# Optimization experiments

Hardware: AMD Instinct MI355X
Metric: run time of the kernel (lower is better)

Reference implementation:

```python
import jax, jax.numpy as jnp
import numpy as np

# Config (Qwen3-4B-like, from ModelConfig defaults in source)
B = 32          # batch = number of decode requests = total_q
H = 32          # num_attention_heads
KVH = 8         # num_key_value_heads
G = H // KVH    # num_kv_groups = 4
D = 128         # head_dim
HID = 2560      # hidden_size
PS = 16         # page_size
MAXP = 128      # max_num_pages per request
NPAGES = B * MAXP   # 4096 pages in pool
MAXKV = MAXP * PS   # 2048
THETA = 5000000.0
EPS = 1e-6


def setup_inputs() -> dict:
    key = jax.random.key(0)
    ks = jax.random.split(key, 12)
    x = jax.random.normal(ks[0], (1, B, HID), dtype=jnp.float32)
    Wq = jax.random.normal(ks[1], (H * D, HID), dtype=jnp.float32) * 0.02
    Wk = jax.random.normal(ks[2], (KVH * D, HID), dtype=jnp.float32) * 0.02
    Wv = jax.random.normal(ks[3], (KVH * D, HID), dtype=jnp.float32) * 0.02
    Wo = jax.random.normal(ks[4], (HID, H * D), dtype=jnp.float32) * 0.02
    q_norm_w = jnp.ones((D,), dtype=jnp.float32)
    k_norm_w = jnp.ones((D,), dtype=jnp.float32)
    K_pool = jax.random.normal(ks[5], (NPAGES, PS, KVH, D), dtype=jnp.float32) * 0.02
    V_pool = jax.random.normal(ks[6], (NPAGES, PS, KVH, D), dtype=jnp.float32) * 0.02
    # each request owns a disjoint contiguous run of pages
    page_indices = jnp.arange(NPAGES, dtype=jnp.int32).reshape(B, MAXP)
    # KV length AFTER writing the single new decode token, in [128, MAXKV]
    lengths_after = jax.random.randint(ks[7], (B,), 128, MAXKV + 1).astype(jnp.int32)
    pos = lengths_after - 1                                  # position of new token
    page_of = page_indices[jnp.arange(B), pos // PS]         # page holding it
    slot_mapping = page_of.astype(jnp.int64) * PS + (pos % PS).astype(jnp.int64)
    # RoPE tables at the new-token positions: cos/sin (1, total_q, 1, D)
    inv_freq = 1.0 / (THETA ** (jnp.arange(0, D, 2, dtype=jnp.float32) / D))
    ang = pos.astype(jnp.float32)[:, None] * inv_freq[None, :]   # (B, D/2)
    ang = jnp.concatenate([ang, ang], axis=-1)                   # (B, D)
    cos = jnp.cos(ang)[None, :, None, :]
    sin = jnp.sin(ang)[None, :, None, :]
    return {"x": x, "cos": cos, "sin": sin, "Wq": Wq, "Wk": Wk, "Wv": Wv,
            "Wo": Wo, "q_norm_w": q_norm_w, "k_norm_w": k_norm_w,
            "K_pool": K_pool, "V_pool": V_pool, "page_indices": page_indices,
            "lengths_after": lengths_after, "slot_mapping": slot_mapping}


def _rmsnorm(x, w):
    xf = x.astype(jnp.float32)
    xf = xf * jax.lax.rsqrt(jnp.mean(xf * xf, axis=-1, keepdims=True) + EPS)
    return (w * xf).astype(x.dtype)


def _rope(x, cos, sin):
    # x: (1, heads, S, D); cos/sin: (1, S, 1, D) -> (1, 1, S, D)
    c = jnp.swapaxes(cos, 1, 2).astype(x.dtype)
    s = jnp.swapaxes(sin, 1, 2).astype(x.dtype)
    x1, x2 = jnp.split(x, 2, axis=-1)
    rot = jnp.concatenate([-x2, x1], axis=-1)
    return x * c + rot * s


def reference(x, cos, sin, Wq, Wk, Wv, Wo, q_norm_w, k_norm_w,
              K_pool, V_pool, page_indices, lengths_after, slot_mapping):
    total_q = x.shape[1]  # == B for decode
    # projections -> (1, heads, total_q, D)
    q = jnp.einsum('bsh,oh->bso', x, Wq).reshape(1, total_q, H, D).transpose(0, 2, 1, 3)
    k = jnp.einsum('bsh,oh->bso', x, Wk).reshape(1, total_q, KVH, D).transpose(0, 2, 1, 3)
    v = jnp.einsum('bsh,oh->bso', x, Wv).reshape(1, total_q, KVH, D).transpose(0, 2, 1, 3)
    # QK-norm (per-head RMSNorm on head_dim), then RoPE
    q = _rope(_rmsnorm(q, q_norm_w), cos, sin)
    k = _rope(_rmsnorm(k, k_norm_w), cos, sin)
    # write new K/V into the page pool (index_copy_ equivalent)
    k_pack = jnp.swapaxes(k[0], 0, 1)  # (total_q, KVH, D)
    v_pack = jnp.swapaxes(v[0], 0, 1)
    Kf = K_pool.reshape(NPAGES * PS, KVH, D).at[slot_mapping].set(k_pack)
    Vf = V_pool.reshape(NPAGES * PS, KVH, D).at[slot_mapping].set(v_pack)
    Kp = Kf.reshape(NPAGES, PS, KVH, D)
    Vp = Vf.reshape(NPAGES, PS, KVH, D)
    # decode path: full page-table gather per request
    flat_idx = page_indices.reshape(-1)
    k_all = Kp[flat_idx].reshape(B, MAXKV, KVH, D)
    v_all = Vp[flat_idx].reshape(B, MAXKV, KVH, D)
    # GQA attention, single query per request; scale = 1/sqrt(D) (SDPA default)
    qg = jnp.swapaxes(q[0], 0, 1).reshape(B, KVH, G, D)  # (B, KVH, G, D)
    scores = jnp.einsum('bkgd,bskd->bkgs', qg, k_all) * (1.0 / np.sqrt(D))
    invalid = jnp.arange(MAXKV)[None, :] >= lengths_after[:, None]  # (B, MAXKV)
    scores = jnp.where(invalid[:, None, None, :], -jnp.inf, scores)
    probs = jax.nn.softmax(scores, axis=-1)
    out = jnp.einsum('bkgs,bskd->bkgd', probs, v_all).reshape(B, H * D)
    y = jnp.einsum('bo,ho->bh', out, Wo)  # o_proj
    return y[None]  # (1, total_q, HID)
```

## Files before the change

kernel.cpp:

```cpp
#include <hip/hip_runtime.h>
#include <math.h>

#define NB    32
#define HIDV  2560
#define HD    128
#define NQH   32
#define NKVH  8

typedef __bf16 bf16x8 __attribute__((ext_vector_type(8)));
typedef float  f32x4  __attribute__((ext_vector_type(4)));

__device__ __forceinline__ unsigned bfpack(float a, float b) {
  unsigned ua = __float_as_uint(a), ub = __float_as_uint(b);
  ua = (ua + 0x7FFFu + ((ua >> 16) & 1u)) >> 16;
  ub = (ub + 0x7FFFu + ((ub >> 16) & 1u)) >> 16;
  return ua | (ub << 16);
}

__device__ __forceinline__ void gemm_body(
    const float* __restrict__ X, const float* __restrict__ W,
    float* __restrict__ P, int N, int K, int f0, int kc0, int slabs, int t,
    unsigned short* Wl, unsigned short* Xl) {
  const int w = t >> 6, l = t & 63;
  const int rA = l & 15, kq = l >> 4;
  f32x4 acc0 = {0.f, 0.f, 0.f, 0.f}, acc1 = {0.f, 0.f, 0.f, 0.f};

  for (int s = 0; s < slabs; ++s) {
    const int kc = kc0 * slabs + s;
    if (s) __syncthreads();
    const float* Wg = W + (size_t)f0 * K + (size_t)kc * 256;
    #pragma unroll
    for (int i = 0; i < 16; ++i) {
      int idx = i * 256 + t;
      int row = idx >> 6, c4 = idx & 63;
      float4 w4 = *(const float4*)(Wg + (size_t)row * K + c4 * 4);
      *(uint2*)((char*)Wl + row * 528 + c4 * 8) =
          make_uint2(bfpack(w4.x, w4.y), bfpack(w4.z, w4.w));
    }
    const float* Xg = X + (size_t)kc * 256;
    #pragma unroll
    for (int i = 0; i < 8; ++i) {
      int idx = i * 256 + t;
      int row = idx >> 6, c4 = idx & 63;
      float4 x4 = *(const float4*)(Xg + (size_t)row * K + c4 * 4);
      *(uint2*)((char*)Xl + row * 528 + c4 * 8) =
          make_uint2(bfpack(x4.x, x4.y), bfpack(x4.z, x4.w));
    }
    __syncthreads();

    const char* pa0 = (const char*)Xl + rA * 528 + kq * 16;
    const char* pa1 = pa0 + 16 * 528;
    const char* pb  = (const char*)Wl + (w * 16 + rA) * 528 + kq * 16;
    #pragma unroll
    for (int ks = 0; ks < 8; ++ks) {
      bf16x8 a0 = *(const bf16x8*)(pa0 + ks * 64);
      bf16x8 a1 = *(const bf16x8*)(pa1 + ks * 64);
      bf16x8 bb = *(const bf16x8*)(pb  + ks * 64);
      acc0 = __builtin_amdgcn_mfma_f32_16x16x32_bf16(a0, bb, acc0, 0, 0, 0);
      acc1 = __builtin_amdgcn_mfma_f32_16x16x32_bf16(a1, bb, acc1, 0, 0, 0);
    }
  }
  const int fcol = f0 + w * 16 + rA;
  float* Pr = P + ((size_t)kc0 * 32) * N + fcol;
  #pragma unroll
  for (int j = 0; j < 4; ++j) {
    int b0 = kq * 4 + j;
    Pr[(size_t)b0 * N]        = acc0[j];
    Pr[(size_t)(b0 + 16) * N] = acc1[j];
  }
}

__global__ __launch_bounds__(256) void qkv_gemm(
    const float* __restrict__ X, const float* __restrict__ Wq,
    const float* __restrict__ Wk, const float* __restrict__ Wv,
    float* __restrict__ qp, float* __restrict__ kp, float* __restrict__ vp) {
  __shared__ __align__(16) unsigned short Wl[64 * 264];
  __shared__ __align__(16) unsigned short Xl[32 * 264];
  const int bx = blockIdx.x;
  const float* W; float* P; int N, f0;
  if (bx < 64)      { W = Wq; P = qp; N = 4096; f0 = bx * 64; }
  else if (bx < 80) { W = Wk; P = kp; N = 1024; f0 = (bx - 64) * 64; }
  else              { W = Wv; P = vp; N = 1024; f0 = (bx - 80) * 64; }
  gemm_body(X, W, P, N, 2560, f0, blockIdx.y, 2, threadIdx.x, Wl, Xl);
}

__global__ __launch_bounds__(256) void o_gemm(
    const float* __restrict__ X, const float* __restrict__ W,
    float* __restrict__ P) {
  __shared__ __align__(16) unsigned short Wl[64 * 264];
  __shared__ __align__(16) unsigned short Xl[32 * 264];
  gemm_body(X, W, P, 2560, 4096, blockIdx.x * 64, blockIdx.y, 2, threadIdx.x, Wl, Xl);
}

__global__ __launch_bounds__(128) void finqkv(
    const float* __restrict__ qp, const float* __restrict__ kp,
    const float* __restrict__ vp, const float* __restrict__ cosb,
    const float* __restrict__ sinb, const float* __restrict__ qw,
    const float* __restrict__ kw, float* __restrict__ qn,
    float* __restrict__ kn, float* __restrict__ vn) {
  const int b = blockIdx.x, h = blockIdx.y, d = threadIdx.x;
  float x = 0.f;
  if (h < 32) {
    #pragma unroll
    for (int c = 0; c < 5; ++c) x += qp[(size_t)(c * 32 + b) * 4096 + h * 128 + d];
  } else if (h < 40) {
    #pragma unroll
    for (int c = 0; c < 5; ++c) x += kp[(size_t)(c * 32 + b) * 1024 + (h - 32) * 128 + d];
  } else {
    #pragma unroll
    for (int c = 0; c < 5; ++c) x += vp[(size_t)(c * 32 + b) * 1024 + (h - 40) * 128 + d];
  }
  if (h >= 40) { vn[((size_t)b * 8 + (h - 40)) * 128 + d] = x; return; }

  __shared__ float red[2];
  __shared__ float sh[128];
  float ss = x * x;
  #pragma unroll
  for (int mk = 1; mk < 64; mk <<= 1) ss += __shfl_xor(ss, mk);
  if ((d & 63) == 0) red[d >> 6] = ss;
  __syncthreads();
  const float inv = rsqrtf((red[0] + red[1]) * (1.f / 128.f) + 1e-6f);
  const float* nw = (h < 32) ? qw : kw;
  const float xn = x * inv * nw[d];
  sh[d] = xn;
  __syncthreads();
  const float rot = (d < 64) ? -sh[d + 64] : sh[d - 64];
  const float o = xn * cosb[b * 128 + d] + rot * sinb[b * 128 + d];
  if (h < 32) qn[((size_t)b * 32 + h) * 128 + d] = o;
  else        kn[((size_t)b * 8 + (h - 32)) * 128 + d] = o;
}

__global__ __launch_bounds__(512) void attn(
    const float* __restrict__ Kp, const float* __restrict__ Vp,
    const float* __restrict__ qn, const float* __restrict__ kn,
    const float* __restrict__ vn, const int* __restrict__ pidx,
    const int* __restrict__ lens, float* __restrict__ ao) {
  const int b = blockIdx.x >> 3, kvh = blockIdx.x & 7;
  const int t = threadIdx.x, w = t >> 6, l = t & 63;
  const int sub = l >> 4, di = (l & 15) * 8;
  __shared__ int pages[128];
  __shared__ float mmS[32][4], msS[32][4];
  __shared__ __align__(16) float maccS[32][4][128];
  if (t < 128) pages[t] = pidx[b * 128 + t];
  __syncthreads();
  const int len = lens[b], lim = len - 1;

  float qf[4][8];
  const float SC = 0.08838834764831845f * 1.4426950408889634f;
  #pragma unroll
  for (int g = 0; g < 4; ++g)
    #pragma unroll
    for (int j = 0; j < 8; ++j)
      qf[g][j] = qn[((size_t)b * 32 + kvh * 4 + g) * 128 + di + j] * SC;

  float m[4], se[4], acc[4][8];
  #pragma unroll
  for (int g = 0; g < 4; ++g) {
    m[g] = -INFINITY; se[g] = 0.f;
    #pragma unroll
    for (int j = 0; j < 8; ++j) acc[g][j] = 0.f;
  }

  const int t0 = w * 4 + sub;
  const int nit = (lim + 31) >> 5;

  auto update = [&](const float (&ck)[8], const float (&cv)[8], bool valid) {
    float s[4];
    #pragma unroll
    for (int g = 0; g < 4; ++g) {
      float d8 = 0.f;
      #pragma unroll
      for (int j = 0; j < 8; ++j) d8 += qf[g][j] * ck[j];
      s[g] = d8;
    }
    #pragma unroll
    for (int mk = 1; mk < 16; mk <<= 1) {
      #pragma unroll
      for (int g = 0; g < 4; ++g) s[g] += __shfl_xor(s[g], mk);
    }
    if (valid) {
      #pragma unroll
      for (int g = 0; g < 4; ++g) {
        const float sg = s[g];
        if (sg > m[g]) {
          const float scf = exp2f(m[g] - sg);
          m[g] = sg;
          se[g] = se[g] * scf + 1.f;
          #pragma unroll
          for (int j = 0; j < 8; ++j) acc[g][j] = acc[g][j] * scf + cv[j];
        } else {
          const float p = exp2f(sg - m[g]);
          se[g] += p;
          #pragma unroll
          for (int j = 0; j < 8; ++j) acc[g][j] += p * cv[j];
        }
      }
    }
  };

  f32x4 ka0, ka1, va0, va1, kb0, kb1, vb0, vb1;
  {
    int tt = min(t0, lim - 1);
    size_t a = ((size_t)pages[tt >> 4] * 16 + (tt & 15)) * 1024 + kvh * 128 + di;
    ka0 = *(const f32x4*)(Kp + a); ka1 = *(const f32x4*)(Kp + a + 4);
    va0 = *(const f32x4*)(Vp + a); va1 = *(const f32x4*)(Vp + a + 4);
  }
  if (nit > 1) {
    int tt = min(32 + t0, lim - 1);
    size_t a = ((size_t)pages[tt >> 4] * 16 + (tt & 15)) * 1024 + kvh * 128 + di;
    kb0 = *(const f32x4*)(Kp + a); kb1 = *(const f32x4*)(Kp + a + 4);
    vb0 = *(const f32x4*)(Vp + a); vb1 = *(const f32x4*)(Vp + a + 4);
  }
  for (int it = 0; it < nit; it += 2) {
    {
      const float ck[8] = {ka0[0], ka0[1], ka0[2], ka0[3], ka1[0], ka1[1], ka1[2], ka1[3]};
      const float cv[8] = {va0[0], va0[1], va0[2], va0[3], va1[0], va1[1], va1[2], va1[3]};
      if (it + 2 < nit) {
        int tt = min((it + 2) * 32 + t0, lim - 1);
        size_t a = ((size_t)pages[tt >> 4] * 16 + (tt & 15)) * 1024 + kvh * 128 + di;
        ka0 = *(const f32x4*)(Kp + a); ka1 = *(const f32x4*)(Kp + a + 4);
        va0 = *(const f32x4*)(Vp + a); va1 = *(const f32x4*)(Vp + a + 4);
      }
      update(ck, cv, it * 32 + t0 < lim);
    }
    if (it + 1 < nit) {
      const float ck[8] = {kb0[0], kb0[1], kb0[2], kb0[3], kb1[0], kb1[1], kb1[2], kb1[3]};
      const float cv[8] = {vb0[0], vb0[1], vb0[2], vb0[3], vb1[0], vb1[1], vb1[2], vb1[3]};
      if (it + 3 < nit) {
        int tt = min((it + 3) * 32 + t0, lim - 1);
        size_t a = ((size_t)pages[tt >> 4] * 16 + (tt & 15)) * 1024 + kvh * 128 + di;
        kb0 = *(const f32x4*)(Kp + a); kb1 = *(const f32x4*)(Kp + a + 4);
        vb0 = *(const f32x4*)(Vp + a); vb1 = *(const f32x4*)(Vp + a + 4);
      }
      update(ck, cv, (it + 1) * 32 + t0 < lim);
    }
  }

  if (w == 0) {
    const float* kr = kn + ((size_t)b * 8 + kvh) * 128 + di;
    const float* vr = vn + ((size_t)b * 8 + kvh) * 128 + di;
    float ck[8], cv[8];
    #pragma unroll
    for (int j = 0; j < 8; ++j) { ck[j] = kr[j]; cv[j] = vr[j]; }
    update(ck, cv, sub == 0);
  }

  const int st = w * 4 + sub;
  if ((l & 15) == 0) {
    #pragma unroll
    for (int g = 0; g < 4; ++g) { mmS[st][g] = m[g]; msS[st][g] = se[g]; }
  }
  #pragma unroll
  for (int g = 0; g < 4; ++g)
    #pragma unroll
    for (int j = 0; j < 8; ++j) maccS[st][g][di + j] = acc[g][j];
  __syncthreads();

  const int g = t >> 7, dd = t & 127;
  float M = -INFINITY;
  #pragma unroll
  for (int s2 = 0; s2 < 32; ++s2) M = fmaxf(M, mmS[s2][g]);
  float den = 0.f, num = 0.f;
  for (int s2 = 0; s2 < 32; ++s2) {
    const float wg = exp2f(mmS[s2][g] - M);
    den += wg * msS[s2][g];
    num += wg * maccS[s2][g][dd];
  }
  ao[((size_t)b * 32 + kvh * 4 + g) * 128 + dd] = num / den;
}

__global__ __launch_bounds__(256) void oreduce(const float* __restrict__ op,
                                               float* __restrict__ y) {
  const int i = blockIdx.x * 256 + threadIdx.x;
  float s = 0.f;
  #pragma unroll
  for (int c = 0; c < 8; ++c) s += op[(size_t)c * (32 * 2560) + i];
  y[i] = s;
}

extern "C" void kernel_launch(void* const* d_in, const int* in_sizes, int n_in,
                              void* d_out, int out_size, void* d_ws, size_t ws_size,
                              hipStream_t stream) {
  const float* x    = (const float*)d_in[0];
  const float* cosb = (const float*)d_in[1];
  const float* sinb = (const float*)d_in[2];
  const float* Wq   = (const float*)d_in[3];
  const float* Wk   = (const float*)d_in[4];
  const float* Wv   = (const float*)d_in[5];
  const float* Wo   = (const float*)d_in[6];
  const float* qw   = (const float*)d_in[7];
  const float* kw   = (const float*)d_in[8];
  const float* Kp   = (const float*)d_in[9];
  const float* Vp   = (const float*)d_in[10];
  const int*   pidx = (const int*)d_in[11];
  const int*   lens = (const int*)d_in[12];
  float* y = (float*)d_out;

  float* ws = (float*)d_ws;
  float* qp = ws;
  float* kp = qp + 655360;
  float* vp = kp + 163840;
  float* qn = vp + 163840;
  float* kn = qn + 131072;
  float* vn = kn + 32768;
  float* ao = vn + 32768;
  float* op = qp;
  (void)in_sizes; (void)n_in; (void)out_size; (void)ws_size;

  qkv_gemm<<<dim3(96, 5), 256, 0, stream>>>(x, Wq, Wk, Wv, qp, kp, vp);
  finqkv<<<dim3(32, 48), 128, 0, stream>>>(qp, kp, vp, cosb, sinb, qw, kw, qn, kn, vn);
  attn<<<256, 512, 0, stream>>>(Kp, Vp, qn, kn, vn, pidx, lens, ao);
  o_gemm<<<dim3(40, 8), 256, 0, stream>>>(ao, Wo, op);
  oreduce<<<320, 256, 0, stream>>>(op, y);
}
```

Before: 97.35 us.

## Split attention across token chunks with all KV heads per block, add merge kernel

The attention kernel now gives each block one request and one of eight interleaved token splits. Each wavefront handles one KV head, so a block reads whole contiguous token rows of the page pool instead of one head's 512-byte slice. Per-split softmax partials (max, sum, accumulator) go to workspace, and a new merge kernel combines them with the freshly computed token's contribution. The aim is better DRAM access locality on the KV stream, at the cost of an extra launch and a partial-result round trip through global memory.

Measured after the change: 104.0 us. +6.9%, slower.

```diff
diff --git a/kernel.cpp b/kernel.cpp
--- a/kernel.cpp
+++ b/kernel.cpp
@@ -130,14 +130,15 @@
   else        kn[((size_t)b * 8 + (h - 32)) * 128 + d] = o;
 }
 
-__global__ __launch_bounds__(512) void attn(
+__global__ __launch_bounds__(512) void attn_main(
     const float* __restrict__ Kp, const float* __restrict__ Vp,
-    const float* __restrict__ qn, const float* __restrict__ kn,
-    const float* __restrict__ vn, const int* __restrict__ pidx,
-    const int* __restrict__ lens, float* __restrict__ ao) {
-  const int b = blockIdx.x >> 3, kvh = blockIdx.x & 7;
+    const float* __restrict__ qn, const int* __restrict__ pidx,
+    const int* __restrict__ lens, float* __restrict__ pm,
+    float* __restrict__ pse, float* __restrict__ pacc) {
+  const int b = blockIdx.x >> 3, s = blockIdx.x & 7;
   const int t = threadIdx.x, w = t >> 6, l = t & 63;
   const int sub = l >> 4, di = (l & 15) * 8;
+  const int kvh = w, tl = sub;
   __shared__ int pages[128];
   __shared__ float mmS[32][4], msS[32][4];
   __shared__ __align__(16) float maccS[32][4][128];
@@ -161,27 +162,26 @@
     for (int j = 0; j < 8; ++j) acc[g][j] = 0.f;
   }
 
-  const int t0 = w * 4 + sub;
-  const int nit = (lim + 31) >> 5;
+  const int nit = (((lim + 3) >> 2) - s + 7) >> 3;
 
   auto update = [&](const float (&ck)[8], const float (&cv)[8], bool valid) {
-    float s[4];
+    float sc[4];
     #pragma unroll
     for (int g = 0; g < 4; ++g) {
       float d8 = 0.f;
       #pragma unroll
       for (int j = 0; j < 8; ++j) d8 += qf[g][j] * ck[j];
-      s[g] = d8;
+      sc[g] = d8;
     }
     #pragma unroll
     for (int mk = 1; mk < 16; mk <<= 1) {
       #pragma unroll
-      for (int g = 0; g < 4; ++g) s[g] += __shfl_xor(s[g], mk);
+      for (int g = 0; g < 4; ++g) sc[g] += __shfl_xor(sc[g], mk);
     }
     if (valid) {
       #pragma unroll
       for (int g = 0; g < 4; ++g) {
-        const float sg = s[g];
+        const float sg = sc[g];
         if (sg > m[g]) {
           const float scf = exp2f(m[g] - sg);
           m[g] = sg;
@@ -198,52 +198,34 @@
     }
   };
 
+#define TOK(IT) (((IT) * 8 + s) * 4 + tl)
+#define LOAD_ST(K0, K1, V0, V1, TOKV) do {                                    \
+    int tt = min((TOKV), lim - 1);                                            \
+    size_t a = ((size_t)pages[tt >> 4] * 16 + (tt & 15)) * 1024               \
+               + kvh * 128 + di;                                              \
+    K0 = *(const f32x4*)(Kp + a); K1 = *(const f32x4*)(Kp + a + 4);           \
+    V0 = *(const f32x4*)(Vp + a); V1 = *(const f32x4*)(Vp + a + 4);           \
+  } while (0)
+
   f32x4 ka0, ka1, va0, va1, kb0, kb1, vb0, vb1;
-  {
-    int tt = min(t0, lim - 1);
-    size_t a = ((size_t)pages[tt >> 4] * 16 + (tt & 15)) * 1024 + kvh * 128 + di;
-    ka0 = *(const f32x4*)(Kp + a); ka1 = *(const f32x4*)(Kp + a + 4);
-    va0 = *(const f32x4*)(Vp + a); va1 = *(const f32x4*)(Vp + a + 4);
-  }
-  if (nit > 1) {
-    int tt = min(32 + t0, lim - 1);
-    size_t a = ((size_t)pages[tt >> 4] * 16 + (tt & 15)) * 1024 + kvh * 128 + di;
-    kb0 = *(const f32x4*)(Kp + a); kb1 = *(const f32x4*)(Kp + a + 4);
-    vb0 = *(const f32x4*)(Vp + a); vb1 = *(const f32x4*)(Vp + a + 4);
-  }
+  LOAD_ST(ka0, ka1, va0, va1, TOK(0));
+  if (nit > 1) LOAD_ST(kb0, kb1, vb0, vb1, TOK(1));
   for (int it = 0; it < nit; it += 2) {
     {
       const float ck[8] = {ka0[0], ka0[1], ka0[2], ka0[3], ka1[0], ka1[1], ka1[2], ka1[3]};
       const float cv[8] = {va0[0], va0[1], va0[2], va0[3], va1[0], va1[1], va1[2], va1[3]};
-      if (it + 2 < nit) {
-        int tt = min((it + 2) * 32 + t0, lim - 1);
-        size_t a = ((size_t)pages[tt >> 4] * 16 + (tt & 15)) * 1024 + kvh * 128 + di;
-        ka0 = *(const f32x4*)(Kp + a); ka1 = *(const f32x4*)(Kp + a + 4);
-        va0 = *(const f32x4*)(Vp + a); va1 = *(const f32x4*)(Vp + a + 4);
-      }
-      update(ck, cv, it * 32 + t0 < lim);
+      if (it + 2 < nit) LOAD_ST(ka0, ka1, va0, va1, TOK(it + 2));
+      update(ck, cv, TOK(it) < lim);
     }
     if (it + 1 < nit) {
       const float ck[8] = {kb0[0], kb0[1], kb0[2], kb0[3], kb1[0], kb1[1], kb1[2], kb1[3]};
       const float cv[8] = {vb0[0], vb0[1], vb0[2], vb0[3], vb1[0], vb1[1], vb1[2], vb1[3]};
-      if (it + 3 < nit) {
-        int tt = min((it + 3) * 32 + t0, lim - 1);
-        size_t a = ((size_t)pages[tt >> 4] * 16 + (tt & 15)) * 1024 + kvh * 128 + di;
-        kb0 = *(const f32x4*)(Kp + a); kb1 = *(const f32x4*)(Kp + a + 4);
-        vb0 = *(const f32x4*)(Vp + a); vb1 = *(const f32x4*)(Vp + a + 4);
-      }
-      update(ck, cv, (it + 1) * 32 + t0 < lim);
-    }
-  }
-
-  if (w == 0) {
-    const float* kr = kn + ((size_t)b * 8 + kvh) * 128 + di;
-    const float* vr = vn + ((size_t)b * 8 + kvh) * 128 + di;
-    float ck[8], cv[8];
-    #pragma unroll
-    for (int j = 0; j < 8; ++j) { ck[j] = kr[j]; cv[j] = vr[j]; }
-    update(ck, cv, sub == 0);
-  }
+      if (it + 3 < nit) LOAD_ST(kb0, kb1, vb0, vb1, TOK(it + 3));
+      update(ck, cv, TOK(it + 1) < lim);
+    }
+  }
+#undef LOAD_ST
+#undef TOK
 
   const int st = w * 4 + sub;
   if ((l & 15) == 0) {
@@ -256,17 +238,60 @@
     for (int j = 0; j < 8; ++j) maccS[st][g][di + j] = acc[g][j];
   __syncthreads();
 
-  const int g = t >> 7, dd = t & 127;
+  #pragma unroll
+  for (int r = 0; r < 8; ++r) {
+    const int idx = r * 512 + t;
+    const int ke = idx >> 9, rem = idx & 511, g = rem >> 7, d = rem & 127;
+    float M = -INFINITY;
+    #pragma unroll
+    for (int q = 0; q < 4; ++q) M = fmaxf(M, mmS[ke * 4 + q][g]);
+    float den = 0.f, num = 0.f;
+    #pragma unroll
+    for (int q = 0; q < 4; ++q) {
+      const float wg = exp2f(mmS[ke * 4 + q][g] - M);
+      den += wg * msS[ke * 4 + q][g];
+      num += wg * maccS[ke * 4 + q][g][d];
+    }
+    const size_t pi = ((size_t)(b * 8 + ke) * 8 + s) * 4 + g;
+    if (d == 0) { pm[pi] = M; pse[pi] = den; }
+    pacc[pi * 128 + d] = num;
+  }
+}
+
+__global__ __launch_bounds__(512) void attn_merge(
+    const float* __restrict__ pm, const float* __restrict__ pse,
+    const float* __restrict__ pacc, const float* __restrict__ qn,
+    const float* __restrict__ kn, const float* __restrict__ vn,
+    float* __restrict__ ao) {
+  const int bk = blockIdx.x, b = bk >> 3, kvh = bk & 7;
+  const int t = threadIdx.x, g = t >> 7, d = t & 127;
+  const float SC = 0.08838834764831845f * 1.4426950408889634f;
+  __shared__ float sred[8];
+
+  float part = qn[((size_t)b * 32 + kvh * 4 + g) * 128 + d] *
+               kn[((size_t)b * 8 + kvh) * 128 + d];
+  #pragma unroll
+  for (int mk = 1; mk < 64; mk <<= 1) part += __shfl_xor(part, mk);
+  if ((t & 63) == 0) sred[t >> 6] = part;
+  __syncthreads();
+  const float snew = (sred[g * 2] + sred[g * 2 + 1]) * SC;
+
   float M = -INFINITY;
   #pragma unroll
-  for (int s2 = 0; s2 < 32; ++s2) M = fmaxf(M, mmS[s2][g]);
+  for (int s = 0; s < 8; ++s) M = fmaxf(M, pm[((size_t)bk * 8 + s) * 4 + g]);
+  M = fmaxf(M, snew);
   float den = 0.f, num = 0.f;
-  for (int s2 = 0; s2 < 32; ++s2) {
-    const float wg = exp2f(mmS[s2][g] - M);
-    den += wg * msS[s2][g];
-    num += wg * maccS[s2][g][dd];
-  }
-  ao[((size_t)b * 32 + kvh * 4 + g) * 128 + dd] = num / den;
+  #pragma unroll
+  for (int s = 0; s < 8; ++s) {
+    const size_t pi = ((size_t)bk * 8 + s) * 4 + g;
+    const float wg = exp2f(pm[pi] - M);
+    den += wg * pse[pi];
+    num += wg * pacc[pi * 128 + d];
+  }
+  const float pn = exp2f(snew - M);
+  den += pn;
+  num += pn * vn[((size_t)b * 8 + kvh) * 128 + d];
+  ao[((size_t)b * 32 + kvh * 4 + g) * 128 + d] = num / den;
 }
 
 __global__ __launch_bounds__(256) void oreduce(const float* __restrict__ op,
@@ -304,12 +329,16 @@
   float* kn = qn + 131072;
   float* vn = kn + 32768;
   float* ao = vn + 32768;
+  float* pm = ao + 131072;
+  float* pse = pm + 8192;
+  float* pacc = pse + 8192;
   float* op = qp;
   (void)in_sizes; (void)n_in; (void)out_size; (void)ws_size;
 
   qkv_gemm<<<dim3(96, 5), 256, 0, stream>>>(x, Wq, Wk, Wv, qp, kp, vp);
   finqkv<<<dim3(32, 48), 128, 0, stream>>>(qp, kp, vp, cosb, sinb, qw, kw, qn, kn, vn);
-  attn<<<256, 512, 0, stream>>>(Kp, Vp, qn, kn, vn, pidx, lens, ao);
+  attn_main<<<256, 512, 0, stream>>>(Kp, Vp, qn, pidx, lens, pm, pse, pacc);
+  attn_merge<<<256, 512, 0, stream>>>(pm, pse, pacc, qn, kn, vn, ao);
   o_gemm<<<dim3(40, 8), 256, 0, stream>>>(ao, Wo, op);
   oreduce<<<320, 256, 0, stream>>>(op, y);
 }
```

## Fuse all five stages into one cooperative persistent kernel with grid syncs

Applied to the files above, without the earlier changes.

Replaces the five separate launches (QKV GEMM, norm/RoPE, attention, O GEMM, reduction) with one cooperative kernel of 256 blocks by 512 threads that separates the stages with grid.sync(). The aim is to remove per-launch overhead and the idle gaps between small kernels. In exchange, the GEMM stages only use half the threads for MFMA work, work units are spread unevenly across 256 blocks (480 and 320 units), and each grid barrier has its own cost. If the cooperative launch fails, the code falls back to the original five launches.

Measured after the change: 228.0 us. 134% more time.

```diff
diff --git a/kernel.cpp b/kernel.cpp
--- a/kernel.cpp
+++ b/kernel.cpp
@@ -1,5 +1,8 @@
 #include <hip/hip_runtime.h>
+#include <hip/hip_cooperative_groups.h>
 #include <math.h>
+
+namespace cg = cooperative_groups;
 
 #define NB    32
 #define HIDV  2560
@@ -67,6 +70,294 @@
     int b0 = kq * 4 + j;
     Pr[(size_t)b0 * N]        = acc0[j];
     Pr[(size_t)(b0 + 16) * N] = acc1[j];
+  }
+}
+
+__device__ __forceinline__ void gemm512(
+    const float* __restrict__ X, const float* __restrict__ W,
+    float* __restrict__ P, int N, int K, int f0, int kc0, int slabs, int t,
+    unsigned short* Wl, unsigned short* Xl) {
+  const bool act = t < 256;
+  const int w = (t >> 6) & 3, l = t & 63;
+  const int rA = l & 15, kq = l >> 4;
+  f32x4 acc0 = {0.f, 0.f, 0.f, 0.f}, acc1 = {0.f, 0.f, 0.f, 0.f};
+
+  for (int s = 0; s < slabs; ++s) {
+    const int kc = kc0 * slabs + s;
+    if (s) __syncthreads();
+    const float* Wg = W + (size_t)f0 * K + (size_t)kc * 256;
+    #pragma unroll
+    for (int i = 0; i < 8; ++i) {
+      int idx = i * 512 + t;
+      int row = idx >> 6, c4 = idx & 63;
+      float4 w4 = *(const float4*)(Wg + (size_t)row * K + c4 * 4);
+      *(uint2*)((char*)Wl + row * 528 + c4 * 8) =
+          make_uint2(bfpack(w4.x, w4.y), bfpack(w4.z, w4.w));
+    }
+    const float* Xg = X + (size_t)kc * 256;
+    #pragma unroll
+    for (int i = 0; i < 4; ++i) {
+      int idx = i * 512 + t;
+      int row = idx >> 6, c4 = idx & 63;
+      float4 x4 = *(const float4*)(Xg + (size_t)row * K + c4 * 4);
+      *(uint2*)((char*)Xl + row * 528 + c4 * 8) =
+          make_uint2(bfpack(x4.x, x4.y), bfpack(x4.z, x4.w));
+    }
+    __syncthreads();
+
+    if (act) {
+      const char* pa0 = (const char*)Xl + rA * 528 + kq * 16;
+      const char* pa1 = pa0 + 16 * 528;
+      const char* pb  = (const char*)Wl + (w * 16 + rA) * 528 + kq * 16;
+      #pragma unroll
+      for (int ks = 0; ks < 8; ++ks) {
+        bf16x8 a0 = *(const bf16x8*)(pa0 + ks * 64);
+        bf16x8 a1 = *(const bf16x8*)(pa1 + ks * 64);
+        bf16x8 bb = *(const bf16x8*)(pb  + ks * 64);
+        acc0 = __builtin_amdgcn_mfma_f32_16x16x32_bf16(a0, bb, acc0, 0, 0, 0);
+        acc1 = __builtin_amdgcn_mfma_f32_16x16x32_bf16(a1, bb, acc1, 0, 0, 0);
+      }
+    }
+  }
+  if (act) {
+    const int fcol = f0 + w * 16 + rA;
+    float* Pr = P + ((size_t)kc0 * 32) * N + fcol;
+    #pragma unroll
+    for (int j = 0; j < 4; ++j) {
+      int b0 = kq * 4 + j;
+      Pr[(size_t)b0 * N]        = acc0[j];
+      Pr[(size_t)(b0 + 16) * N] = acc1[j];
+    }
+  }
+}
+
+__global__ __launch_bounds__(512, 2) void fused(
+    const float* __restrict__ x, const float* __restrict__ cosb,
+    const float* __restrict__ sinb, const float* __restrict__ Wq,
+    const float* __restrict__ Wk, const float* __restrict__ Wv,
+    const float* __restrict__ Wo, const float* __restrict__ qw,
+    const float* __restrict__ kw, const float* __restrict__ Kp,
+    const float* __restrict__ Vp, const int* __restrict__ pidx,
+    const int* __restrict__ lens, float* __restrict__ qp,
+    float* __restrict__ kp, float* __restrict__ vp, float* __restrict__ qn,
+    float* __restrict__ kn, float* __restrict__ vn, float* __restrict__ ao,
+    float* __restrict__ op, float* __restrict__ y) {
+  cg::grid_group grid = cg::this_grid();
+  __shared__ __align__(16) char smem[67072];
+  const int bid = blockIdx.x, t = threadIdx.x;
+
+  for (int u = bid; u < 480; u += 256) {
+    __syncthreads();
+    unsigned short* Wl = (unsigned short*)smem;
+    unsigned short* Xl = (unsigned short*)(smem + 33792);
+    const int bx = u / 5, kc = u - bx * 5;
+    const float* W; float* P; int N, f0;
+    if (bx < 64)      { W = Wq; P = qp; N = 4096; f0 = bx * 64; }
+    else if (bx < 80) { W = Wk; P = kp; N = 1024; f0 = (bx - 64) * 64; }
+    else              { W = Wv; P = vp; N = 1024; f0 = (bx - 80) * 64; }
+    gemm512(x, W, P, N, 2560, f0, kc, 2, t, Wl, Xl);
+  }
+  grid.sync();
+
+  {
+    float* red = (float*)smem;
+    float* sh  = (float*)(smem + 32);
+    for (int u = bid; u < 384; u += 256) {
+      const int b = u / 12, qd = u - (u / 12) * 12;
+      const int hl = t >> 7, d = t & 127;
+      const int H = qd * 4 + hl;
+      __syncthreads();
+      if (qd >= 10) {
+        float xv = 0.f;
+        #pragma unroll
+        for (int c = 0; c < 5; ++c)
+          xv += vp[(size_t)(c * 32 + b) * 1024 + (H - 40) * 128 + d];
+        vn[((size_t)b * 8 + (H - 40)) * 128 + d] = xv;
+      } else {
+        const bool isq = qd < 8;
+        float xx = 0.f;
+        if (isq) {
+          #pragma unroll
+          for (int c = 0; c < 5; ++c)
+            xx += qp[(size_t)(c * 32 + b) * 4096 + H * 128 + d];
+        } else {
+          #pragma unroll
+          for (int c = 0; c < 5; ++c)
+            xx += kp[(size_t)(c * 32 + b) * 1024 + (H - 32) * 128 + d];
+        }
+        float ss = xx * xx;
+        #pragma unroll
+        for (int mk = 1; mk < 64; mk <<= 1) ss += __shfl_xor(ss, mk);
+        if ((t & 63) == 0) red[t >> 6] = ss;
+        __syncthreads();
+        const float inv =
+            rsqrtf((red[hl * 2] + red[hl * 2 + 1]) * (1.f / 128.f) + 1e-6f);
+        const float xn = xx * inv * (isq ? qw[d] : kw[d]);
+        sh[hl * 128 + d] = xn;
+        __syncthreads();
+        const float rp = sh[hl * 128 + (d ^ 64)];
+        const float o = xn * cosb[b * 128 + d] +
+                        ((d < 64) ? -rp : rp) * sinb[b * 128 + d];
+        if (isq) qn[((size_t)b * 32 + H) * 128 + d] = o;
+        else     kn[((size_t)b * 8 + (H - 32)) * 128 + d] = o;
+      }
+    }
+  }
+  grid.sync();
+
+  {
+    int* pages = (int*)smem;
+    float (*mmS)[4] = (float(*)[4])(smem + 512);
+    float (*msS)[4] = (float(*)[4])(smem + 1024);
+    float (*maccS)[4][128] = (float(*)[4][128])(smem + 1536);
+    const int b = bid >> 3, kvh = bid & 7;
+    const int w = t >> 6, l = t & 63;
+    const int sub = l >> 4, di = (l & 15) * 8;
+    if (t < 128) pages[t] = pidx[b * 128 + t];
+    __syncthreads();
+    const int len = lens[b], lim = len - 1;
+
+    float qf[4][8];
+    const float SC = 0.08838834764831845f * 1.4426950408889634f;
+    #pragma unroll
+    for (int g = 0; g < 4; ++g)
+      #pragma unroll
+      for (int j = 0; j < 8; ++j)
+        qf[g][j] = qn[((size_t)b * 32 + kvh * 4 + g) * 128 + di + j] * SC;
+
+    float m[4], se[4], acc[4][8];
+    #pragma unroll
+    for (int g = 0; g < 4; ++g) {
+      m[g] = -INFINITY; se[g] = 0.f;
+      #pragma unroll
+      for (int j = 0; j < 8; ++j) acc[g][j] = 0.f;
+    }
+
+    const int t0 = w * 4 + sub;
+    const int nit = (lim + 31) >> 5;
+
+    auto update = [&](const float (&ck)[8], const float (&cv)[8], bool valid) {
+      float s[4];
+      #pragma unroll
+      for (int g = 0; g < 4; ++g) {
+        float d8 = 0.f;
+        #pragma unroll
+        for (int j = 0; j < 8; ++j) d8 += qf[g][j] * ck[j];
+        s[g] = d8;
+      }
+      #pragma unroll
+      for (int mk = 1; mk < 16; mk <<= 1) {
+        #pragma unroll
+        for (int g = 0; g < 4; ++g) s[g] += __shfl_xor(s[g], mk);
+      }
+      if (valid) {
+        #pragma unroll
+        for (int g = 0; g < 4; ++g) {
+          const float sg = s[g];
+          if (sg > m[g]) {
+            const float scf = exp2f(m[g] - sg);
+            m[g] = sg;
+            se[g] = se[g] * scf + 1.f;
+            #pragma unroll
+            for (int j = 0; j < 8; ++j) acc[g][j] = acc[g][j] * scf + cv[j];
+          } else {
+            const float p = exp2f(sg - m[g]);
+            se[g] += p;
+            #pragma unroll
+            for (int j = 0; j < 8; ++j) acc[g][j] += p * cv[j];
+          }
+        }
+      }
+    };
+
+    f32x4 ka0, ka1, va0, va1, kb0, kb1, vb0, vb1;
+    {
+      int tt = min(t0, lim - 1);
+      size_t a = ((size_t)pages[tt >> 4] * 16 + (tt & 15)) * 1024 + kvh * 128 + di;
+      ka0 = *(const f32x4*)(Kp + a); ka1 = *(const f32x4*)(Kp + a + 4);
+      va0 = *(const f32x4*)(Vp + a); va1 = *(const f32x4*)(Vp + a + 4);
+    }
+    if (nit > 1) {
+      int tt = min(32 + t0, lim - 1);
+      size_t a = ((size_t)pages[tt >> 4] * 16 + (tt & 15)) * 1024 + kvh * 128 + di;
+      kb0 = *(const f32x4*)(Kp + a); kb1 = *(const f32x4*)(Kp + a + 4);
+      vb0 = *(const f32x4*)(Vp + a); vb1 = *(const f32x4*)(Vp + a + 4);
+    }
+    for (int it = 0; it < nit; it += 2) {
+      {
+        const float ck[8] = {ka0[0], ka0[1], ka0[2], ka0[3], ka1[0], ka1[1], ka1[2], ka1[3]};
+        const float cv[8] = {va0[0], va0[1], va0[2], va0[3], va1[0], va1[1], va1[2], va1[3]};
+        if (it + 2 < nit) {
+          int tt = min((it + 2) * 32 + t0, lim - 1);
+          size_t a = ((size_t)pages[tt >> 4] * 16 + (tt & 15)) * 1024 + kvh * 128 + di;
+          ka0 = *(const f32x4*)(Kp + a); ka1 = *(const f32x4*)(Kp + a + 4);
+          va0 = *(const f32x4*)(Vp + a); va1 = *(const f32x4*)(Vp + a + 4);
+        }
+        update(ck, cv, it * 32 + t0 < lim);
+      }
+      if (it + 1 < nit) {
+        const float ck[8] = {kb0[0], kb0[1], kb0[2], kb0[3], kb1[0], kb1[1], kb1[2], kb1[3]};
+        const float cv[8] = {vb0[0], vb0[1], vb0[2], vb0[3], vb1[0], vb1[1], vb1[2], vb1[3]};
+        if (it + 3 < nit) {
+          int tt = min((it + 3) * 32 + t0, lim - 1);
+          size_t a = ((size_t)pages[tt >> 4] * 16 + (tt & 15)) * 1024 + kvh * 128 + di;
+          kb0 = *(const f32x4*)(Kp + a); kb1 = *(const f32x4*)(Kp + a + 4);
+          vb0 = *(const f32x4*)(Vp + a); vb1 = *(const f32x4*)(Vp + a + 4);
+        }
+        update(ck, cv, (it + 1) * 32 + t0 < lim);
+      }
+    }
+
+    if (w == 0) {
+      const float* kr = kn + ((size_t)b * 8 + kvh) * 128 + di;
+      const float* vr = vn + ((size_t)b * 8 + kvh) * 128 + di;
+      float ck[8], cv[8];
+      #pragma unroll
+      for (int j = 0; j < 8; ++j) { ck[j] = kr[j]; cv[j] = vr[j]; }
+      update(ck, cv, sub == 0);
+    }
+
+    const int st = w * 4 + sub;
+    if ((l & 15) == 0) {
+      #pragma unroll
+      for (int g = 0; g < 4; ++g) { mmS[st][g] = m[g]; msS[st][g] = se[g]; }
+    }
+    #pragma unroll
+    for (int g = 0; g < 4; ++g)
+      #pragma unroll
+      for (int j = 0; j < 8; ++j) maccS[st][g][di + j] = acc[g][j];
+    __syncthreads();
+
+    const int g = t >> 7, dd = t & 127;
+    float M = -INFINITY;
+    #pragma unroll
+    for (int s2 = 0; s2 < 32; ++s2) M = fmaxf(M, mmS[s2][g]);
+    float den = 0.f, num = 0.f;
+    for (int s2 = 0; s2 < 32; ++s2) {
+      const float wg = exp2f(mmS[s2][g] - M);
+      den += wg * msS[s2][g];
+      num += wg * maccS[s2][g][dd];
+    }
+    ao[((size_t)b * 32 + kvh * 4 + g) * 128 + dd] = num / den;
+  }
+  grid.sync();
+
+  for (int u = bid; u < 320; u += 256) {
+    __syncthreads();
+    unsigned short* Wl = (unsigned short*)smem;
+    unsigned short* Xl = (unsigned short*)(smem + 33792);
+    gemm512(ao, Wo, op, 2560, 4096, (u >> 3) * 64, u & 7, 2, t, Wl, Xl);
+  }
+  grid.sync();
+
+  {
+    const int i = bid * 512 + t;
+    if (i < 81920) {
+      float s = 0.f;
+      #pragma unroll
+      for (int c = 0; c < 8; ++c) s += op[(size_t)c * 81920 + i];
+      y[i] = s;
+    }
   }
 }
 
@@ -307,9 +598,16 @@
   float* op = qp;
   (void)in_sizes; (void)n_in; (void)out_size; (void)ws_size;
 
-  qkv_gemm<<<dim3(96, 5), 256, 0, stream>>>(x, Wq, Wk, Wv, qp, kp, vp);
-  finqkv<<<dim3(32, 48), 128, 0, stream>>>(qp, kp, vp, cosb, sinb, qw, kw, qn, kn, vn);
-  attn<<<256, 512, 0, stream>>>(Kp, Vp, qn, kn, vn, pidx, lens, ao);
-  o_gemm<<<dim3(40, 8), 256, 0, stream>>>(ao, Wo, op);
-  oreduce<<<320, 256, 0, stream>>>(op, y);
-}
+  void* args[] = {&x, &cosb, &sinb, &Wq, &Wk, &Wv, &Wo, &qw, &kw, &Kp, &Vp,
+                  &pidx, &lens, &qp, &kp, &vp, &qn, &kn, &vn, &ao, &op, &y};
+  hipError_t e = hipLaunchCooperativeKernel((void*)fused, dim3(256), dim3(512),
+                                            args, 0, stream);
+  if (e != hipSuccess) {
+    (void)hipGetLastError();
+    qkv_gemm<<<dim3(96, 5), 256, 0, stream>>>(x, Wq, Wk, Wv, qp, kp, vp);
+    finqkv<<<dim3(32, 48), 128, 0, stream>>>(qp, kp, vp, cosb, sinb, qw, kw, qn, kn, vn);
+    attn<<<256, 512, 0, stream>>>(Kp, Vp, qn, kn, vn, pidx, lens, ao);
+    o_gemm<<<dim3(40, 8), 256, 0, stream>>>(ao, Wo, op);
+    oreduce<<<320, 256, 0, stream>>>(op, y);
+  }
+}
```

## Fuse split-K reductions and QK norm/RoPE into GEMMs via last-block atomic counters

Applied to the files above, without the earlier changes.

The QKV GEMM and the o_proj GEMM now each finish their own split-K reduction. Every block bumps a per-output-tile atomic counter, and the last block to arrive sums the partials. For QKV it also applies the RMSNorm and RoPE epilogue, and for o_proj it writes the final output. This drops the separate finqkv and oreduce launches and their launch gaps, at the cost of a memset launch, threadfences, and serialized tail work on the last-arriving blocks.

Result: slower. 213.6 us (+119.4%).

```diff
diff --git a/kernel.cpp b/kernel.cpp
--- a/kernel.cpp
+++ b/kernel.cpp
@@ -70,64 +70,104 @@
   }
 }
 
-__global__ __launch_bounds__(256) void qkv_gemm(
+__global__ __launch_bounds__(256) void qkv_gemm_f(
     const float* __restrict__ X, const float* __restrict__ Wq,
     const float* __restrict__ Wk, const float* __restrict__ Wv,
-    float* __restrict__ qp, float* __restrict__ kp, float* __restrict__ vp) {
+    const float* __restrict__ cosb, const float* __restrict__ sinb,
+    const float* __restrict__ qw, const float* __restrict__ kw,
+    float* __restrict__ qp, float* __restrict__ kp, float* __restrict__ vp,
+    float* __restrict__ qn, float* __restrict__ kn, float* __restrict__ vn,
+    int* __restrict__ cnt) {
   __shared__ __align__(16) unsigned short Wl[64 * 264];
   __shared__ __align__(16) unsigned short Xl[32 * 264];
-  const int bx = blockIdx.x;
+  __shared__ int oldv;
+  __shared__ float red2[4];
+  __shared__ float sh2[2][128];
+  const int bx = blockIdx.x, t = threadIdx.x;
   const float* W; float* P; int N, f0;
   if (bx < 64)      { W = Wq; P = qp; N = 4096; f0 = bx * 64; }
   else if (bx < 80) { W = Wk; P = kp; N = 1024; f0 = (bx - 64) * 64; }
   else              { W = Wv; P = vp; N = 1024; f0 = (bx - 80) * 64; }
-  gemm_body(X, W, P, N, 2560, f0, blockIdx.y, 2, threadIdx.x, Wl, Xl);
-}
-
-__global__ __launch_bounds__(256) void o_gemm(
+  gemm_body(X, W, P, N, 2560, f0, blockIdx.y, 2, t, Wl, Xl);
+
+  const int id = (bx < 64) ? (bx >> 1)
+               : (bx < 80) ? 32 + ((bx - 64) >> 1)
+                           : 40 + ((bx - 80) >> 1);
+  __threadfence();
+  __syncthreads();
+  if (t == 0) oldv = atomicAdd(&cnt[id], 1);
+  __syncthreads();
+  if (oldv != 9) return;
+  __threadfence();
+
+  const int r = t >> 7, d = t & 127;
+  if (id >= 40) {
+    const int h = id - 40;
+    #pragma unroll
+    for (int i = 0; i < 16; ++i) {
+      const int b = i * 2 + r;
+      float xv = 0.f;
+      #pragma unroll
+      for (int c = 0; c < 5; ++c)
+        xv += vp[(size_t)(c * 32 + b) * 1024 + h * 128 + d];
+      vn[((size_t)b * 8 + h) * 128 + d] = xv;
+    }
+    return;
+  }
+  const bool isq = id < 32;
+  const int h = isq ? id : id - 32;
+  const float* src = isq ? qp : kp;
+  const float* nw  = isq ? qw : kw;
+  const int stride = isq ? 4096 : 1024;
+  for (int i = 0; i < 16; ++i) {
+    const int b = i * 2 + r;
+    float xx = 0.f;
+    #pragma unroll
+    for (int c = 0; c < 5; ++c)
+      xx += src[(size_t)(c * 32 + b) * stride + h * 128 + d];
+    float ss = xx * xx;
+    #pragma unroll
+    for (int mk = 1; mk < 64; mk <<= 1) ss += __shfl_xor(ss, mk);
+    if ((t & 63) == 0) red2[t >> 6] = ss;
+    __syncthreads();
+    const float inv = rsqrtf((red2[r * 2] + red2[r * 2 + 1]) * (1.f / 128.f) + 1e-6f);
+    const float xn = xx * inv * nw[d];
+    sh2[r][d] = xn;
+    __syncthreads();
+    const float rp = sh2[r][d ^ 64];
+    const float o = xn * cosb[b * 128 + d] + ((d < 64) ? -rp : rp) * sinb[b * 128 + d];
+    if (isq) qn[((size_t)b * 32 + h) * 128 + d] = o;
+    else     kn[((size_t)b * 8 + h) * 128 + d] = o;
+    __syncthreads();
+  }
+}
+
+__global__ __launch_bounds__(256) void o_gemm_f(
     const float* __restrict__ X, const float* __restrict__ W,
-    float* __restrict__ P) {
+    float* __restrict__ op, float* __restrict__ y, int* __restrict__ cnt) {
   __shared__ __align__(16) unsigned short Wl[64 * 264];
   __shared__ __align__(16) unsigned short Xl[32 * 264];
-  gemm_body(X, W, P, 2560, 4096, blockIdx.x * 64, blockIdx.y, 2, threadIdx.x, Wl, Xl);
-}
-
-__global__ __launch_bounds__(128) void finqkv(
-    const float* __restrict__ qp, const float* __restrict__ kp,
-    const float* __restrict__ vp, const float* __restrict__ cosb,
-    const float* __restrict__ sinb, const float* __restrict__ qw,
-    const float* __restrict__ kw, float* __restrict__ qn,
-    float* __restrict__ kn, float* __restrict__ vn) {
-  const int b = blockIdx.x, h = blockIdx.y, d = threadIdx.x;
-  float x = 0.f;
-  if (h < 32) {
-    #pragma unroll
-    for (int c = 0; c < 5; ++c) x += qp[(size_t)(c * 32 + b) * 4096 + h * 128 + d];
-  } else if (h < 40) {
-    #pragma unroll
-    for (int c = 0; c < 5; ++c) x += kp[(size_t)(c * 32 + b) * 1024 + (h - 32) * 128 + d];
-  } else {
-    #pragma unroll
-    for (int c = 0; c < 5; ++c) x += vp[(size_t)(c * 32 + b) * 1024 + (h - 40) * 128 + d];
-  }
-  if (h >= 40) { vn[((size_t)b * 8 + (h - 40)) * 128 + d] = x; return; }
-
-  __shared__ float red[2];
-  __shared__ float sh[128];
-  float ss = x * x;
-  #pragma unroll
-  for (int mk = 1; mk < 64; mk <<= 1) ss += __shfl_xor(ss, mk);
-  if ((d & 63) == 0) red[d >> 6] = ss;
-  __syncthreads();
-  const float inv = rsqrtf((red[0] + red[1]) * (1.f / 128.f) + 1e-6f);
-  const float* nw = (h < 32) ? qw : kw;
-  const float xn = x * inv * nw[d];
-  sh[d] = xn;
-  __syncthreads();
-  const float rot = (d < 64) ? -sh[d + 64] : sh[d - 64];
-  const float o = xn * cosb[b * 128 + d] + rot * sinb[b * 128 + d];
-  if (h < 32) qn[((size_t)b * 32 + h) * 128 + d] = o;
-  else        kn[((size_t)b * 8 + (h - 32)) * 128 + d] = o;
+  __shared__ int oldv;
+  const int bx = blockIdx.x, t = threadIdx.x;
+  const int f0 = bx * 64;
+  gemm_body(X, W, op, 2560, 4096, f0, blockIdx.y, 2, t, Wl, Xl);
+
+  __threadfence();
+  __syncthreads();
+  if (t == 0) oldv = atomicAdd(&cnt[48 + bx], 1);
+  __syncthreads();
+  if (oldv != 7) return;
+  __threadfence();
+
+  #pragma unroll
+  for (int i = 0; i < 8; ++i) {
+    const int o = i * 256 + t, b = o >> 6, f = o & 63;
+    float s = 0.f;
+    #pragma unroll
+    for (int c = 0; c < 8; ++c)
+      s += op[(size_t)(c * 32 + b) * 2560 + f0 + f];
+    y[b * 2560 + f0 + f] = s;
+  }
 }
 
 __global__ __launch_bounds__(512) void attn(
@@ -269,15 +309,6 @@
   ao[((size_t)b * 32 + kvh * 4 + g) * 128 + dd] = num / den;
 }
 
-__global__ __launch_bounds__(256) void oreduce(const float* __restrict__ op,
-                                               float* __restrict__ y) {
-  const int i = blockIdx.x * 256 + threadIdx.x;
-  float s = 0.f;
-  #pragma unroll
-  for (int c = 0; c < 8; ++c) s += op[(size_t)c * (32 * 2560) + i];
-  y[i] = s;
-}
-
 extern "C" void kernel_launch(void* const* d_in, const int* in_sizes, int n_in,
                               void* d_out, int out_size, void* d_ws, size_t ws_size,
                               hipStream_t stream) {
@@ -304,12 +335,13 @@
   float* kn = qn + 131072;
   float* vn = kn + 32768;
   float* ao = vn + 32768;
+  int*   cnt = (int*)(ao + 131072);
   float* op = qp;
   (void)in_sizes; (void)n_in; (void)out_size; (void)ws_size;
 
-  qkv_gemm<<<dim3(96, 5), 256, 0, stream>>>(x, Wq, Wk, Wv, qp, kp, vp);
-  finqkv<<<dim3(32, 48), 128, 0, stream>>>(qp, kp, vp, cosb, sinb, qw, kw, qn, kn, vn);
+  hipMemsetAsync(cnt, 0, 88 * sizeof(int), stream);
+  qkv_gemm_f<<<dim3(96, 5), 256, 0, stream>>>(x, Wq, Wk, Wv, cosb, sinb, qw, kw,
+                                              qp, kp, vp, qn, kn, vn, cnt);
   attn<<<256, 512, 0, stream>>>(Kp, Vp, qn, kn, vn, pidx, lens, ao);
-  o_gemm<<<dim3(40, 8), 256, 0, stream>>>(ao, Wo, op);
-  oreduce<<<320, 256, 0, stream>>>(op, y);
-}
+  o_gemm_f<<<dim3(40, 8), 256, 0, stream>>>(ao, Wo, op, y, cnt);
+}
```
